# Optimization experiments

Measured on AMD Instinct MI355X. Metric: run time of the kernel, lower is better.

## Reference

```python
import jax, jax.numpy as jnp
import numpy as np

B, S, D, UNITS = 8, 2048, 512, 512

def setup_inputs() -> dict:
    key = jax.random.key(0)
    k1, k2, k3, k4 = jax.random.split(key, 4)
    scale = 1.0 / np.sqrt(D)
    return {
        "x": jax.random.normal(k1, (B, S, D), dtype=jnp.float32),
        "Wq": jax.random.normal(k2, (D, UNITS), dtype=jnp.float32) * scale,
        "Wk": jax.random.normal(k3, (D, UNITS), dtype=jnp.float32) * scale,
        "Wv": jax.random.normal(k4, (D, UNITS), dtype=jnp.float32) * scale,
    }

def reference(x, Wq, Wk, Wv):
    # Q, K, V: [B, S, units]
    Q = jnp.einsum('bsd,du->bsu', x, Wq)
    Km = jnp.einsum('bsd,du->bsu', x, Wk)
    V = jnp.einsum('bsd,du->bsu', x, Wv)
    d_k = jnp.asarray(Wq.shape[-1], dtype=x.dtype)
    # scores: [B, S, S]
    scores = jnp.einsum('bqu,bku->bqk', Q, Km) / jnp.sqrt(d_k)
    attn = jax.nn.softmax(scores, axis=-1)
    return jnp.einsum('bqk,bku->bqu', attn, V)
```

## Files before the change

kernel.cpp:

```cpp
#include <hip/hip_runtime.h>

typedef __attribute__((ext_vector_type(8))) __bf16 bf16x8;
typedef __attribute__((ext_vector_type(4))) float f32x4;
typedef unsigned short u16;
typedef unsigned int u32;

#define VMCNT(n) asm volatile("s_waitcnt vmcnt(" #n ")" ::: "memory")

__device__ __forceinline__ u16 f2bf(float f) {
  union { float f; u32 u; } v; v.f = f;
  u32 r = v.u + 0x7FFFu + ((v.u >> 16) & 1u);
  return (u16)(r >> 16);
}
__device__ __forceinline__ float fexp2(float x) {
  float r; asm("v_exp_f32 %0, %1" : "=v"(r) : "v"(x)); return r;
}

__global__ __launch_bounds__(256) void cast_x_kernel(const float* __restrict__ x,
                                                     u16* __restrict__ xb, int n4) {
  int i = blockIdx.x * 256 + threadIdx.x;
  if (i >= n4) return;
  float4 v = reinterpret_cast<const float4*>(x)[i];
  ushort4 o;
  o.x = f2bf(v.x); o.y = f2bf(v.y); o.z = f2bf(v.z); o.w = f2bf(v.w);
  reinterpret_cast<ushort4*>(xb)[i] = o;
}

__global__ __launch_bounds__(1024) void transpose_w_kernel(const float* __restrict__ Wq,
                                                           const float* __restrict__ Wk,
                                                           const float* __restrict__ Wv,
                                                           u16* __restrict__ Wt) {
  const float* src = blockIdx.z == 0 ? Wq : (blockIdx.z == 1 ? Wk : Wv);
  u16* dst = Wt + (size_t)blockIdx.z * 512 * 512;
  __shared__ float tile[32][33];
  int u0 = blockIdx.x * 32, d0 = blockIdx.y * 32;
  tile[threadIdx.y][threadIdx.x] = src[(d0 + threadIdx.y) * 512 + u0 + threadIdx.x];
  __syncthreads();
  dst[(u0 + threadIdx.y) * 512 + d0 + threadIdx.x] = f2bf(tile[threadIdx.x][threadIdx.y]);
}

__global__ __launch_bounds__(256) void qkv_kernel(const u16* __restrict__ Xb,
                                                  const u16* __restrict__ Wt3,
                                                  u16* __restrict__ Q, u16* __restrict__ K,
                                                  u16* __restrict__ Vt2) {
  __shared__ u16 As[3][128 * 32], Bs[3][128 * 32];
  const int bm = blockIdx.y * 128;
  const int bn = blockIdx.x * 128;
  const int z = blockIdx.z;
  const u16* A = Xb + (size_t)bm * 512;
  const u16* Bt = Wt3 + (size_t)z * 512 * 512 + (size_t)bn * 512;

  const int t = threadIdx.x;
  const int lane = t & 63;
  const int w = t >> 6;
  const int wr = w >> 1, wc = w & 1;
  const int la = lane & 15;
  const int q = lane >> 4;
  f32x4 acc[4][4] = {};

  auto stage = [&](int buf, int kt) {
    const int k0 = kt * 32;
#pragma unroll
    for (int it = 0; it < 2; ++it) {
      int c = it * 256 + t, row = c >> 2;
      int col = ((c & 3) ^ ((row >> 1) & 3)) << 3;
      __builtin_amdgcn_global_load_lds(
          (const __attribute__((address_space(1))) void*)(A + (size_t)row * 512 + k0 + col),
          (__attribute__((address_space(3))) void*)(&As[buf][c * 8]), 16, 0, 0);
    }
#pragma unroll
    for (int it = 0; it < 2; ++it) {
      int c = it * 256 + t, row = c >> 2;
      int col = ((c & 3) ^ ((row >> 1) & 3)) << 3;
      __builtin_amdgcn_global_load_lds(
          (const __attribute__((address_space(1))) void*)(Bt + (size_t)row * 512 + k0 + col),
          (__attribute__((address_space(3))) void*)(&Bs[buf][c * 8]), 16, 0, 0);
    }
  };

  auto body = [&](int buf) {
    bf16x8 a[4], b[4];
#pragma unroll
    for (int i = 0; i < 4; ++i) {
      int row = wr * 64 + i * 16 + la;
      a[i] = *reinterpret_cast<const bf16x8*>(&As[buf][row * 32 + ((q ^ ((row >> 1) & 3)) << 3)]);
    }
#pragma unroll
    for (int j = 0; j < 4; ++j) {
      int row = wc * 64 + j * 16 + la;
      b[j] = *reinterpret_cast<const bf16x8*>(&Bs[buf][row * 32 + ((q ^ ((row >> 1) & 3)) << 3)]);
    }
    __builtin_amdgcn_s_setprio(1);
#pragma unroll
    for (int i = 0; i < 4; ++i)
#pragma unroll
      for (int j = 0; j < 4; ++j)
        acc[i][j] = __builtin_amdgcn_mfma_f32_16x16x32_bf16(a[i], b[j], acc[i][j], 0, 0, 0);
    __builtin_amdgcn_s_setprio(0);
  };

  stage(0, 0); stage(1, 1);
  int cb = 0, sb = 2;
  for (int kt = 0; kt < 14; ++kt) {
    VMCNT(4);
    __builtin_amdgcn_s_barrier();
    stage(sb, kt + 2);
    body(cb);
    cb = (cb == 2) ? 0 : cb + 1;
    sb = (sb == 2) ? 0 : sb + 1;
  }
  VMCNT(4); __builtin_amdgcn_s_barrier(); body(2);
  VMCNT(0); __builtin_amdgcn_s_barrier(); body(0);

  const int r0 = q * 4, cn = lane & 15;
  if (z < 2) {
    u16* out = (z == 0) ? Q : K;
#pragma unroll
    for (int i = 0; i < 4; ++i)
#pragma unroll
      for (int j = 0; j < 4; ++j)
#pragma unroll
        for (int r = 0; r < 4; ++r) {
          int m = bm + 64 * wr + 16 * i + r0 + r;
          int n = bn + 64 * wc + 16 * j + cn;
          out[(size_t)m * 512 + n] = f2bf(acc[i][j][r]);
        }
  } else {
#pragma unroll
    for (int i = 0; i < 4; ++i)
#pragma unroll
      for (int j = 0; j < 4; ++j)
#pragma unroll
        for (int r = 0; r < 4; ++r) {
          int m = bm + 64 * wr + 16 * i + r0 + r;
          int u = bn + 64 * wc + 16 * j + cn;
          int b = m >> 11, s = m & 2047;
          Vt2[(((size_t)b * 64 + (s >> 5)) * 512 + u) * 32 + (s & 31)] = f2bf(acc[i][j][r]);
        }
  }
}

__global__ __launch_bounds__(512) void scores8_kernel(const u16* __restrict__ Q,
                                                      const u16* __restrict__ K,
                                                      u16* __restrict__ S2) {
  __shared__ u16 ring[4][2][256 * 32];
  const int bb = blockIdx.x;
  const int bm = blockIdx.y * 256;
  const int bn = blockIdx.z * 256;
  const u16* Aq = Q + (size_t)(bb * 2048 + bm) * 512;
  const u16* Bk = K + (size_t)(bb * 2048 + bn) * 512;

  const int t = threadIdx.x;
  const int lane = t & 63;
  const int wid = t >> 6;
  const int wm = wid >> 2, wn = wid & 3;
  const int la = lane & 15;
  const int q = lane >> 4;

  f32x4 acc[8][4] = {};

  auto stage = [&](int kt) {
    const int r = kt & 3;
    const int koff = kt * 32;
#pragma unroll
    for (int half = 0; half < 2; ++half) {
      int c = half * 512 + t;
      int row = c >> 2;
      int col = ((c & 3) ^ ((row >> 1) & 3)) << 3;
      __builtin_amdgcn_global_load_lds(
          (const __attribute__((address_space(1))) void*)(Aq + (size_t)row * 512 + koff + col),
          (__attribute__((address_space(3))) void*)(&ring[r][0][c * 8]), 16, 0, 0);
      __builtin_amdgcn_global_load_lds(
          (const __attribute__((address_space(1))) void*)(Bk + (size_t)row * 512 + koff + col),
          (__attribute__((address_space(3))) void*)(&ring[r][1][c * 8]), 16, 0, 0);
    }
  };

  auto body = [&](int kt) {
    const int r = kt & 3;
    const u16* At = ring[r][0];
    const u16* Bt = ring[r][1];
    bf16x8 bfr[4], afr[8];
#pragma unroll
    for (int j = 0; j < 4; ++j) {
      int row = wn * 64 + j * 16 + la;
      bfr[j] = *reinterpret_cast<const bf16x8*>(Bt + row * 32 + ((q ^ ((row >> 1) & 3)) << 3));
    }
#pragma unroll
    for (int i = 0; i < 8; ++i) {
      int row = wm * 128 + i * 16 + la;
      afr[i] = *reinterpret_cast<const bf16x8*>(At + row * 32 + ((q ^ ((row >> 1) & 3)) << 3));
    }
    __builtin_amdgcn_s_setprio(1);
#pragma unroll
    for (int i = 0; i < 8; ++i)
#pragma unroll
      for (int j = 0; j < 4; ++j)
        acc[i][j] = __builtin_amdgcn_mfma_f32_16x16x32_bf16(afr[i], bfr[j], acc[i][j], 0, 0, 0);
    __builtin_amdgcn_s_setprio(0);
  };

  stage(0); stage(1); stage(2);
  for (int kt = 0; kt < 13; ++kt) {
    VMCNT(8);
    __builtin_amdgcn_s_barrier();
    stage(kt + 3);
    body(kt);
  }
  VMCNT(8); __builtin_amdgcn_s_barrier(); body(13);
  VMCNT(4); __builtin_amdgcn_s_barrier(); body(14);
  VMCNT(0); __builtin_amdgcn_s_barrier(); body(15);

  const float scale = 0.06375872127f;
  const int r0h = q * 4;
#pragma unroll
  for (int i = 0; i < 8; ++i)
#pragma unroll
    for (int j = 0; j < 4; ++j) {
      int n = bn + wn * 64 + j * 16;
      int kt_j = n >> 5;
      int ke_j = (n & 31) + la;
      u16* dst = S2 + ((size_t)(bb * 64 + kt_j) * 2048) * 32 + ke_j;
#pragma unroll
      for (int r = 0; r < 4; ++r) {
        int m = bm + wm * 128 + i * 16 + r0h + r;
        dst[(size_t)m * 32] = f2bf(fexp2(acc[i][j][r] * scale));
      }
    }
}

__global__ __launch_bounds__(256) void pv_kernel(const u16* __restrict__ S2,
                                                 const u16* __restrict__ Vt2,
                                                 float* __restrict__ out) {
  __shared__ u16 As[4][128 * 32], Bs[4][128 * 32];
  __shared__ float larr[128];
  const int id = blockIdx.x;
  const int b = id & 7;
  const int local = id >> 3;
  const int bn = (local & 3) * 128;
  const int bm = (local >> 2) * 128;

  const u16* A2 = S2 + ((size_t)b * 64 * 2048 + (size_t)bm) * 32;
  const u16* B2 = Vt2 + ((size_t)b * 64 * 512 + (size_t)bn) * 32;

  const int t = threadIdx.x;
  const int lane = t & 63;
  const int w = t >> 6;
  const int wr = w >> 1, wc = w & 1;
  const int la = lane & 15;
  const int q = lane >> 4;
  f32x4 acc[4][4] = {};
  float lacc[4] = {0.f, 0.f, 0.f, 0.f};

  auto stage = [&](int kt) {
    const int buf = kt & 3;
    const u16* At = A2 + (size_t)kt * 65536;
    const u16* Bt = B2 + (size_t)kt * 16384;
#pragma unroll
    for (int it = 0; it < 2; ++it) {
      int c = it * 256 + t, row = c >> 2;
      int col = ((c & 3) ^ ((row >> 1) & 3)) << 3;
      __builtin_amdgcn_global_load_lds(
          (const __attribute__((address_space(1))) void*)(At + row * 32 + col),
          (__attribute__((address_space(3))) void*)(&As[buf][c * 8]), 16, 0, 0);
    }
#pragma unroll
    for (int it = 0; it < 2; ++it) {
      int c = it * 256 + t, row = c >> 2;
      int col = ((c & 3) ^ ((row >> 1) & 3)) << 3;
      __builtin_amdgcn_global_load_lds(
          (const __attribute__((address_space(1))) void*)(Bt + row * 32 + col),
          (__attribute__((address_space(3))) void*)(&Bs[buf][c * 8]), 16, 0, 0);
    }
  };

  auto body = [&](int kt) {
    const int buf = kt & 3;
    bf16x8 a[4], bb[4];
#pragma unroll
    for (int i = 0; i < 4; ++i) {
      int row = wr * 64 + i * 16 + la;
      a[i] = *reinterpret_cast<const bf16x8*>(&As[buf][row * 32 + ((q ^ ((row >> 1) & 3)) << 3)]);
    }
    if (wc == 0) {
#pragma unroll
      for (int i = 0; i < 4; ++i) {
        float ls = 0.f;
#pragma unroll
        for (int e = 0; e < 8; ++e) ls += (float)a[i][e];
        lacc[i] += ls;
      }
    }
#pragma unroll
    for (int j = 0; j < 4; ++j) {
      int row = wc * 64 + j * 16 + la;
      bb[j] = *reinterpret_cast<const bf16x8*>(&Bs[buf][row * 32 + ((q ^ ((row >> 1) & 3)) << 3)]);
    }
    __builtin_amdgcn_s_setprio(1);
#pragma unroll
    for (int i = 0; i < 4; ++i)
#pragma unroll
      for (int j = 0; j < 4; ++j)
        acc[i][j] = __builtin_amdgcn_mfma_f32_16x16x32_bf16(a[i], bb[j], acc[i][j], 0, 0, 0);
    __builtin_amdgcn_s_setprio(0);
  };

  stage(0); stage(1); stage(2);
  for (int kt = 0; kt < 61; ++kt) {
    VMCNT(8);
    __builtin_amdgcn_s_barrier();
    stage(kt + 3);
    body(kt);
  }
  VMCNT(8); __builtin_amdgcn_s_barrier(); body(61);
  VMCNT(4); __builtin_amdgcn_s_barrier(); body(62);
  VMCNT(0); __builtin_amdgcn_s_barrier(); body(63);

  float l[4];
#pragma unroll
  for (int i = 0; i < 4; ++i) {
    l[i] = lacc[i];
    l[i] += __shfl_xor(l[i], 16);
    l[i] += __shfl_xor(l[i], 32);
  }
  if (wc == 0 && q == 0) {
#pragma unroll
    for (int i = 0; i < 4; ++i) larr[wr * 64 + i * 16 + la] = l[i];
  }
  __syncthreads();

  float* C = out + ((size_t)b * 2048 + bm) * 512;
  const int r0 = q * 4, cn = lane & 15;
  float inv[4][4];
#pragma unroll
  for (int i = 0; i < 4; ++i)
#pragma unroll
    for (int r = 0; r < 4; ++r)
      inv[i][r] = 1.0f / larr[wr * 64 + i * 16 + r0 + r];
#pragma unroll
  for (int i = 0; i < 4; ++i)
#pragma unroll
    for (int j = 0; j < 4; ++j)
#pragma unroll
      for (int r = 0; r < 4; ++r) {
        int m = 64 * wr + 16 * i + r0 + r;
        int n = bn + 64 * wc + 16 * j + cn;
        C[(size_t)m * 512 + n] = acc[i][j][r] * inv[i][r];
      }
}

extern "C" void kernel_launch(void* const* d_in, const int* in_sizes, int n_in,
                              void* d_out, int out_size, void* d_ws, size_t ws_size,
                              hipStream_t stream) {
  const float* x  = (const float*)d_in[0];
  const float* Wq = (const float*)d_in[1];
  const float* Wk = (const float*)d_in[2];
  const float* Wv = (const float*)d_in[3];
  float* out = (float*)d_out;

  char* p = (char*)d_ws;
  u16* Xb = (u16*)p;            p += (size_t)16384 * 512 * 2;
  u16* Wt = (u16*)p;            p += (size_t)3 * 512 * 512 * 2;
  u16* Q  = (u16*)p;            p += (size_t)16384 * 512 * 2;
  u16* K  = (u16*)p;            p += (size_t)16384 * 512 * 2;
  u16* Vt2 = (u16*)p;           p += (size_t)16384 * 512 * 2;
  u16* S2 = (u16*)p;

  cast_x_kernel<<<dim3(8192), dim3(256), 0, stream>>>(x, Xb, 16384 * 512 / 4);
  transpose_w_kernel<<<dim3(16, 16, 3), dim3(32, 32), 0, stream>>>(Wq, Wk, Wv, Wt);
  qkv_kernel<<<dim3(4, 128, 3), dim3(256), 0, stream>>>(Xb, Wt, Q, K, Vt2);
  scores8_kernel<<<dim3(8, 8, 8), dim3(512), 0, stream>>>(Q, K, S2);
  pv_kernel<<<dim3(512), dim3(256), 0, stream>>>(S2, Vt2, out);
}
```

Before: 149.9 us.

## Enlarge PV tile to 256x128 with 512 threads and 64-deep K stages

Result: no change. 152.3 us (+1.5%).

```diff
diff --git a/kernel.cpp b/kernel.cpp
--- a/kernel.cpp
+++ b/kernel.cpp
@@ -229,92 +229,103 @@
     }
 }
 
-__global__ __launch_bounds__(256) void pv_kernel(const u16* __restrict__ S2,
+__global__ __launch_bounds__(512) void pv_kernel(const u16* __restrict__ S2,
                                                  const u16* __restrict__ Vt2,
                                                  float* __restrict__ out) {
-  __shared__ u16 As[4][128 * 32], Bs[4][128 * 32];
-  __shared__ float larr[128];
+  __shared__ u16 As[3][2][256 * 32];
+  __shared__ u16 Bs[3][2][128 * 32];
+  __shared__ float larr[256];
   const int id = blockIdx.x;
   const int b = id & 7;
   const int local = id >> 3;
   const int bn = (local & 3) * 128;
-  const int bm = (local >> 2) * 128;
+  const int bm = (local >> 2) * 256;
 
   const u16* A2 = S2 + ((size_t)b * 64 * 2048 + (size_t)bm) * 32;
   const u16* B2 = Vt2 + ((size_t)b * 64 * 512 + (size_t)bn) * 32;
 
   const int t = threadIdx.x;
   const int lane = t & 63;
-  const int w = t >> 6;
-  const int wr = w >> 1, wc = w & 1;
+  const int wid = t >> 6;
+  const int wm = wid >> 1;
+  const int wn = wid & 1;
   const int la = lane & 15;
   const int q = lane >> 4;
+
   f32x4 acc[4][4] = {};
   float lacc[4] = {0.f, 0.f, 0.f, 0.f};
 
-  auto stage = [&](int kt) {
-    const int buf = kt & 3;
-    const u16* At = A2 + (size_t)kt * 65536;
-    const u16* Bt = B2 + (size_t)kt * 16384;
+  auto stage = [&](int s) {
+    const int buf = s % 3;
+#pragma unroll
+    for (int it = 0; it < 4; ++it) {
+      int c = it * 512 + t;
+      int h = c >> 10;
+      int idx = c & 1023;
+      int row = idx >> 2;
+      int col = ((c & 3) ^ ((row >> 1) & 3)) << 3;
+      __builtin_amdgcn_global_load_lds(
+          (const __attribute__((address_space(1))) void*)(A2 + (size_t)(2 * s + h) * 65536 + row * 32 + col),
+          (__attribute__((address_space(3))) void*)(&As[buf][0][c * 8]), 16, 0, 0);
+    }
 #pragma unroll
     for (int it = 0; it < 2; ++it) {
-      int c = it * 256 + t, row = c >> 2;
-      int col = ((c & 3) ^ ((row >> 1) & 3)) << 3;
-      __builtin_amdgcn_global_load_lds(
-          (const __attribute__((address_space(1))) void*)(At + row * 32 + col),
-          (__attribute__((address_space(3))) void*)(&As[buf][c * 8]), 16, 0, 0);
-    }
-#pragma unroll
-    for (int it = 0; it < 2; ++it) {
-      int c = it * 256 + t, row = c >> 2;
-      int col = ((c & 3) ^ ((row >> 1) & 3)) << 3;
-      __builtin_amdgcn_global_load_lds(
-          (const __attribute__((address_space(1))) void*)(Bt + row * 32 + col),
-          (__attribute__((address_space(3))) void*)(&Bs[buf][c * 8]), 16, 0, 0);
-    }
-  };
-
-  auto body = [&](int kt) {
-    const int buf = kt & 3;
-    bf16x8 a[4], bb[4];
-#pragma unroll
-    for (int i = 0; i < 4; ++i) {
-      int row = wr * 64 + i * 16 + la;
-      a[i] = *reinterpret_cast<const bf16x8*>(&As[buf][row * 32 + ((q ^ ((row >> 1) & 3)) << 3)]);
-    }
-    if (wc == 0) {
+      int c = it * 512 + t;
+      int h = c >> 9;
+      int idx = c & 511;
+      int row = idx >> 2;
+      int col = ((c & 3) ^ ((row >> 1) & 3)) << 3;
+      __builtin_amdgcn_global_load_lds(
+          (const __attribute__((address_space(1))) void*)(B2 + (size_t)(2 * s + h) * 16384 + row * 32 + col),
+          (__attribute__((address_space(3))) void*)(&Bs[buf][0][c * 8]), 16, 0, 0);
+    }
+  };
+
+  auto body = [&](int s) {
+    const int buf = s % 3;
+#pragma unroll
+    for (int h = 0; h < 2; ++h) {
+      const u16* Ah = &As[buf][h][0];
+      const u16* Bh = &Bs[buf][h][0];
+      bf16x8 a[4], bb[4];
 #pragma unroll
       for (int i = 0; i < 4; ++i) {
-        float ls = 0.f;
-#pragma unroll
-        for (int e = 0; e < 8; ++e) ls += (float)a[i][e];
-        lacc[i] += ls;
-      }
-    }
-#pragma unroll
-    for (int j = 0; j < 4; ++j) {
-      int row = wc * 64 + j * 16 + la;
-      bb[j] = *reinterpret_cast<const bf16x8*>(&Bs[buf][row * 32 + ((q ^ ((row >> 1) & 3)) << 3)]);
-    }
-    __builtin_amdgcn_s_setprio(1);
-#pragma unroll
-    for (int i = 0; i < 4; ++i)
-#pragma unroll
-      for (int j = 0; j < 4; ++j)
-        acc[i][j] = __builtin_amdgcn_mfma_f32_16x16x32_bf16(a[i], bb[j], acc[i][j], 0, 0, 0);
-    __builtin_amdgcn_s_setprio(0);
-  };
-
-  stage(0); stage(1); stage(2);
-  for (int kt = 0; kt < 61; ++kt) {
-    VMCNT(8);
+        int row = wm * 64 + i * 16 + la;
+        a[i] = *reinterpret_cast<const bf16x8*>(Ah + row * 32 + ((q ^ ((row >> 1) & 3)) << 3));
+      }
+      if (wn == 0) {
+#pragma unroll
+        for (int i = 0; i < 4; ++i) {
+          float ls = 0.f;
+#pragma unroll
+          for (int e = 0; e < 8; ++e) ls += (float)a[i][e];
+          lacc[i] += ls;
+        }
+      }
+#pragma unroll
+      for (int j = 0; j < 4; ++j) {
+        int row = wn * 64 + j * 16 + la;
+        bb[j] = *reinterpret_cast<const bf16x8*>(Bh + row * 32 + ((q ^ ((row >> 1) & 3)) << 3));
+      }
+      __builtin_amdgcn_s_setprio(1);
+#pragma unroll
+      for (int i = 0; i < 4; ++i)
+#pragma unroll
+        for (int j = 0; j < 4; ++j)
+          acc[i][j] = __builtin_amdgcn_mfma_f32_16x16x32_bf16(a[i], bb[j], acc[i][j], 0, 0, 0);
+      __builtin_amdgcn_s_setprio(0);
+    }
+  };
+
+  stage(0); stage(1);
+  for (int s = 0; s < 30; ++s) {
+    VMCNT(6);
     __builtin_amdgcn_s_barrier();
-    stage(kt + 3);
-    body(kt);
-  }
-  VMCNT(8); __builtin_amdgcn_s_barrier(); body(61);
-  VMCNT(4); __builtin_amdgcn_s_barrier(); body(62);
-  VMCNT(0); __builtin_amdgcn_s_barrier(); body(63);
+    stage(s + 2);
+    body(s);
+  }
+  VMCNT(6); __builtin_amdgcn_s_barrier(); body(30);
+  VMCNT(0); __builtin_amdgcn_s_barrier(); body(31);
 
   float l[4];
 #pragma unroll
@@ -323,9 +334,9 @@
     l[i] += __shfl_xor(l[i], 16);
     l[i] += __shfl_xor(l[i], 32);
   }
-  if (wc == 0 && q == 0) {
-#pragma unroll
-    for (int i = 0; i < 4; ++i) larr[wr * 64 + i * 16 + la] = l[i];
+  if (wn == 0 && q == 0) {
+#pragma unroll
+    for (int i = 0; i < 4; ++i) larr[wm * 64 + i * 16 + la] = l[i];
   }
   __syncthreads();
 
@@ -336,15 +347,15 @@
   for (int i = 0; i < 4; ++i)
 #pragma unroll
     for (int r = 0; r < 4; ++r)
-      inv[i][r] = 1.0f / larr[wr * 64 + i * 16 + r0 + r];
+      inv[i][r] = 1.0f / larr[wm * 64 + i * 16 + r0 + r];
 #pragma unroll
   for (int i = 0; i < 4; ++i)
 #pragma unroll
     for (int j = 0; j < 4; ++j)
 #pragma unroll
       for (int r = 0; r < 4; ++r) {
-        int m = 64 * wr + 16 * i + r0 + r;
-        int n = bn + 64 * wc + 16 * j + cn;
+        int m = wm * 64 + 16 * i + r0 + r;
+        int n = bn + 64 * wn + 16 * j + cn;
         C[(size_t)m * 512 + n] = acc[i][j][r] * inv[i][r];
       }
 }
@@ -370,5 +381,5 @@
   transpose_w_kernel<<<dim3(16, 16, 3), dim3(32, 32), 0, stream>>>(Wq, Wk, Wv, Wt);
   qkv_kernel<<<dim3(4, 128, 3), dim3(256), 0, stream>>>(Xb, Wt, Q, K, Vt2);
   scores8_kernel<<<dim3(8, 8, 8), dim3(512), 0, stream>>>(Q, K, S2);
-  pv_kernel<<<dim3(512), dim3(256), 0, stream>>>(S2, Vt2, out);
-}
+  pv_kernel<<<dim3(256), dim3(512), 0, stream>>>(S2, Vt2, out);
+}
```

## Use 512-thread blocks with 8 waves and 3-stage pipeline in pv_kernel

Applied to the files above, without the earlier changes.

New measurement: 142.6 us. 1.05x faster.

```diff
diff --git a/kernel.cpp b/kernel.cpp
--- a/kernel.cpp
+++ b/kernel.cpp
@@ -229,10 +229,10 @@
     }
 }
 
-__global__ __launch_bounds__(256) void pv_kernel(const u16* __restrict__ S2,
-                                                 const u16* __restrict__ Vt2,
-                                                 float* __restrict__ out) {
-  __shared__ u16 As[4][128 * 32], Bs[4][128 * 32];
+__global__ __launch_bounds__(512, 4) void pv_kernel(const u16* __restrict__ S2,
+                                                    const u16* __restrict__ Vt2,
+                                                    float* __restrict__ out) {
+  __shared__ u16 As[3][128 * 32], Bs[3][128 * 32];
   __shared__ float larr[128];
   const int id = blockIdx.x;
   const int b = id & 7;
@@ -245,46 +245,41 @@
 
   const int t = threadIdx.x;
   const int lane = t & 63;
-  const int w = t >> 6;
-  const int wr = w >> 1, wc = w & 1;
+  const int wid = t >> 6;
+  const int wm = wid >> 1;
+  const int wn = wid & 1;
   const int la = lane & 15;
   const int q = lane >> 4;
-  f32x4 acc[4][4] = {};
-  float lacc[4] = {0.f, 0.f, 0.f, 0.f};
+
+  f32x4 acc[2][4] = {};
+  float lacc[2] = {0.f, 0.f};
 
   auto stage = [&](int kt) {
-    const int buf = kt & 3;
+    const int buf = kt % 3;
     const u16* At = A2 + (size_t)kt * 65536;
     const u16* Bt = B2 + (size_t)kt * 16384;
-#pragma unroll
-    for (int it = 0; it < 2; ++it) {
-      int c = it * 256 + t, row = c >> 2;
-      int col = ((c & 3) ^ ((row >> 1) & 3)) << 3;
-      __builtin_amdgcn_global_load_lds(
-          (const __attribute__((address_space(1))) void*)(At + row * 32 + col),
-          (__attribute__((address_space(3))) void*)(&As[buf][c * 8]), 16, 0, 0);
-    }
-#pragma unroll
-    for (int it = 0; it < 2; ++it) {
-      int c = it * 256 + t, row = c >> 2;
-      int col = ((c & 3) ^ ((row >> 1) & 3)) << 3;
-      __builtin_amdgcn_global_load_lds(
-          (const __attribute__((address_space(1))) void*)(Bt + row * 32 + col),
-          (__attribute__((address_space(3))) void*)(&Bs[buf][c * 8]), 16, 0, 0);
-    }
+    int c = t;
+    int row = c >> 2;
+    int col = ((c & 3) ^ ((row >> 1) & 3)) << 3;
+    __builtin_amdgcn_global_load_lds(
+        (const __attribute__((address_space(1))) void*)(At + row * 32 + col),
+        (__attribute__((address_space(3))) void*)(&As[buf][c * 8]), 16, 0, 0);
+    __builtin_amdgcn_global_load_lds(
+        (const __attribute__((address_space(1))) void*)(Bt + row * 32 + col),
+        (__attribute__((address_space(3))) void*)(&Bs[buf][c * 8]), 16, 0, 0);
   };
 
   auto body = [&](int kt) {
-    const int buf = kt & 3;
-    bf16x8 a[4], bb[4];
-#pragma unroll
-    for (int i = 0; i < 4; ++i) {
-      int row = wr * 64 + i * 16 + la;
+    const int buf = kt % 3;
+    bf16x8 a[2], bb[4];
+#pragma unroll
+    for (int i = 0; i < 2; ++i) {
+      int row = wm * 32 + i * 16 + la;
       a[i] = *reinterpret_cast<const bf16x8*>(&As[buf][row * 32 + ((q ^ ((row >> 1) & 3)) << 3)]);
     }
-    if (wc == 0) {
-#pragma unroll
-      for (int i = 0; i < 4; ++i) {
+    if (wn == 0) {
+#pragma unroll
+      for (int i = 0; i < 2; ++i) {
         float ls = 0.f;
 #pragma unroll
         for (int e = 0; e < 8; ++e) ls += (float)a[i][e];
@@ -293,58 +288,57 @@
     }
 #pragma unroll
     for (int j = 0; j < 4; ++j) {
-      int row = wc * 64 + j * 16 + la;
+      int row = wn * 64 + j * 16 + la;
       bb[j] = *reinterpret_cast<const bf16x8*>(&Bs[buf][row * 32 + ((q ^ ((row >> 1) & 3)) << 3)]);
     }
     __builtin_amdgcn_s_setprio(1);
 #pragma unroll
-    for (int i = 0; i < 4; ++i)
+    for (int i = 0; i < 2; ++i)
 #pragma unroll
       for (int j = 0; j < 4; ++j)
         acc[i][j] = __builtin_amdgcn_mfma_f32_16x16x32_bf16(a[i], bb[j], acc[i][j], 0, 0, 0);
     __builtin_amdgcn_s_setprio(0);
   };
 
-  stage(0); stage(1); stage(2);
-  for (int kt = 0; kt < 61; ++kt) {
-    VMCNT(8);
+  stage(0); stage(1);
+  for (int kt = 0; kt < 62; ++kt) {
+    VMCNT(2);
     __builtin_amdgcn_s_barrier();
-    stage(kt + 3);
+    stage(kt + 2);
     body(kt);
   }
-  VMCNT(8); __builtin_amdgcn_s_barrier(); body(61);
-  VMCNT(4); __builtin_amdgcn_s_barrier(); body(62);
+  VMCNT(2); __builtin_amdgcn_s_barrier(); body(62);
   VMCNT(0); __builtin_amdgcn_s_barrier(); body(63);
 
-  float l[4];
-#pragma unroll
-  for (int i = 0; i < 4; ++i) {
+  float l[2];
+#pragma unroll
+  for (int i = 0; i < 2; ++i) {
     l[i] = lacc[i];
     l[i] += __shfl_xor(l[i], 16);
     l[i] += __shfl_xor(l[i], 32);
   }
-  if (wc == 0 && q == 0) {
-#pragma unroll
-    for (int i = 0; i < 4; ++i) larr[wr * 64 + i * 16 + la] = l[i];
+  if (wn == 0 && q == 0) {
+#pragma unroll
+    for (int i = 0; i < 2; ++i) larr[wm * 32 + i * 16 + la] = l[i];
   }
   __syncthreads();
 
   float* C = out + ((size_t)b * 2048 + bm) * 512;
   const int r0 = q * 4, cn = lane & 15;
-  float inv[4][4];
-#pragma unroll
-  for (int i = 0; i < 4; ++i)
+  float inv[2][4];
+#pragma unroll
+  for (int i = 0; i < 2; ++i)
 #pragma unroll
     for (int r = 0; r < 4; ++r)
-      inv[i][r] = 1.0f / larr[wr * 64 + i * 16 + r0 + r];
-#pragma unroll
-  for (int i = 0; i < 4; ++i)
+      inv[i][r] = 1.0f / larr[wm * 32 + i * 16 + r0 + r];
+#pragma unroll
+  for (int i = 0; i < 2; ++i)
 #pragma unroll
     for (int j = 0; j < 4; ++j)
 #pragma unroll
       for (int r = 0; r < 4; ++r) {
-        int m = 64 * wr + 16 * i + r0 + r;
-        int n = bn + 64 * wc + 16 * j + cn;
+        int m = wm * 32 + 16 * i + r0 + r;
+        int n = bn + 64 * wn + 16 * j + cn;
         C[(size_t)m * 512 + n] = acc[i][j][r] * inv[i][r];
       }
 }
@@ -370,5 +364,5 @@
   transpose_w_kernel<<<dim3(16, 16, 3), dim3(32, 32), 0, stream>>>(Wq, Wk, Wv, Wt);
   qkv_kernel<<<dim3(4, 128, 3), dim3(256), 0, stream>>>(Xb, Wt, Q, K, Vt2);
   scores8_kernel<<<dim3(8, 8, 8), dim3(512), 0, stream>>>(Q, K, S2);
-  pv_kernel<<<dim3(512), dim3(256), 0, stream>>>(S2, Vt2, out);
-}
+  pv_kernel<<<dim3(512), dim3(512), 0, stream>>>(S2, Vt2, out);
+}
```
